# Kernel tuning notes

Measured on AMD Instinct MI355X. Metric: run time of the kernel, lower is better.

The kernel has to match this reference:

```python
import jax, jax.numpy as jnp
import numpy as np

DN = ('NCHW', 'OIHW', 'NCHW')
EPS = 1e-5


def _conv(x, w, b, stride, pad):
    y = jax.lax.conv_general_dilated(x, w, (stride, stride), ((pad, pad), (pad, pad)), dimension_numbers=DN)
    return y + b[None, :, None, None]


def _convT(x, w, b):
    # PyTorch ConvTranspose2d(k=3, stride=2, padding=1, output_padding=1)
    # weight w: [in, out, kh, kw] -> flip spatial, swap in/out -> OIHW
    wt = jnp.flip(w, (2, 3)).transpose(1, 0, 2, 3)
    y = jax.lax.conv_general_dilated(x, wt, (1, 1), ((1, 2), (1, 2)), lhs_dilation=(2, 2), dimension_numbers=DN)
    return y + b[None, :, None, None]


def _inorm(x):
    # InstanceNorm2d, affine=False, biased variance (num_features arg unused since no affine)
    m = x.mean((2, 3), keepdims=True)
    v = ((x - m) ** 2).mean((2, 3), keepdims=True)
    return (x - m) / jnp.sqrt(v + EPS)


def _lrelu(x):
    return jnp.where(x >= 0, x, 0.2 * x)


def _refpad(x):
    return jnp.pad(x, ((0, 0), (0, 0), (1, 1), (1, 1)), mode='reflect')


def _backbone(image, w1, b1, w2, b2, w3, b3, wt, bt, w4, b4):
    x = _lrelu(_inorm(_conv(_refpad(image), w1, b1, 1, 0)))   # [B,32,H,W]
    x = _lrelu(_inorm(_conv(x, w2, b2, 2, 1)))                 # [B,64,H/2,W/2]
    x = _lrelu(_inorm(_conv(x, w3, b3, 2, 1)))                 # [B,128,H/4,W/4]
    x = _lrelu(_inorm(_convT(x, wt, bt)))                      # [B,256,H/2,W/2]
    x = jnp.tanh(_conv(_refpad(x), w4, b4, 1, 0))              # [B,512,H/2,W/2]
    return x


def _style_codes(x, seg):
    # nearest interpolation of seg to (h,w): src_idx = floor(dst * H / h)
    B, C, h, w = x.shape
    H, W = seg.shape[2], seg.shape[3]
    rows = (np.arange(h) * H) // h
    cols = (np.arange(w) * W) // w
    seg_ds = seg[:, :, rows][:, :, :, cols]                    # [B,L,h,w]
    m = (seg_ds != 0).astype(x.dtype)
    sums = jnp.einsum('bchw,blhw->blc', x, m)                  # segment sums
    counts = m.sum((2, 3))[..., None]                          # [B,L,1]
    return jnp.where(counts > 0, sums / jnp.maximum(counts, 1.0), 0.0)


def setup_inputs():
    key = jax.random.key(0)
    ks = jax.random.split(key, 8)
    B, H, W, L = 8, 256, 256, 19
    image = jax.random.normal(ks[0], (B, 3, H, W), jnp.float32)
    labels = jax.random.randint(ks[1], (B, H, W), 0, L)
    seg = jax.nn.one_hot(labels, L, axis=1, dtype=jnp.float32)  # one-hot semantic map
    def w(k, shape):
        return jax.random.normal(k, shape, jnp.float32) * 0.05
    return {
        'image': image, 'seg': seg,
        'w1': w(ks[2], (32, 3, 3, 3)), 'b1': jnp.zeros(32, jnp.float32),
        'w2': w(ks[3], (64, 32, 3, 3)), 'b2': jnp.zeros(64, jnp.float32),
        'w3': w(ks[4], (128, 64, 3, 3)), 'b3': jnp.zeros(128, jnp.float32),
        'wt': w(ks[5], (128, 256, 3, 3)), 'bt': jnp.zeros(256, jnp.float32),
        'w4': w(ks[6], (512, 256, 3, 3)), 'b4': jnp.zeros(512, jnp.float32),
    }


def reference(image, seg, w1, b1, w2, b2, w3, b3, wt, bt, w4, b4):
    x = _backbone(image, w1, b1, w2, b2, w3, b3, wt, bt, w4, b4)
    return _style_codes(x, seg)  # [B, label_nc, 512]
```

## Files before the change

### kernel.cpp

```cpp
#include <hip/hip_runtime.h>
#include <hip/hip_bf16.h>
#include <math.h>

typedef __attribute__((ext_vector_type(8))) short bf16x8;
typedef __attribute__((ext_vector_type(8))) unsigned short u16x8;
typedef __attribute__((ext_vector_type(4))) float f32x4;
typedef __attribute__((ext_vector_type(2))) long longx2;

#define OFF_X1   0ull
#define OFF_XQ8  0ull
#define OFF_X2   34080768ull
#define OFF_X3   51386368ull
#define OFF_Y4   60039168ull
#define OFF_WB8  127148032ull
#define OFF_WB2  129507328ull
#define OFF_WB3  129548288ull
#define OFF_WBT  129695744ull
#define OFF_ST1  130744320ull
#define OFF_ST2  130746368ull
#define OFF_ST3  130750464ull
#define OFF_ST4  130758656ull
#define OFF_SUMS 130775040ull
#define OFF_CNT  131086336ull
#define OFF_LAB  131117664ull
#define OFF_DWS  131641952ull
#define OFF_WSM  132166240ull
#define OFF_ST5  132690528ull
#define OFF_CB   132706912ull

__device__ __forceinline__ float bfu2f(unsigned short u) {
  return __builtin_bit_cast(float, ((unsigned)u) << 16);
}
__device__ __forceinline__ unsigned short f2bfu(float f) {
  __hip_bfloat16 h = __float2bfloat16(f);
  return __builtin_bit_cast(unsigned short, h);
}
__device__ __forceinline__ void gload_lds16(const void* g, void* l) {
  __builtin_amdgcn_global_load_lds(
      (const __attribute__((address_space(1))) unsigned int*)g,
      (__attribute__((address_space(3))) unsigned int*)l, 16, 0, 0);
}
template <bool HI>
__device__ __forceinline__ int cvtpk8(float a, float b, int old) {
  return __builtin_amdgcn_cvt_pk_fp8_f32(a, b, old, HI);
}
template <int SEL>
__device__ __forceinline__ float cvtf8(int v) {
  return __builtin_amdgcn_cvt_f32_fp8(v, SEL);
}

#define WAITV(N) asm volatile("s_waitcnt vmcnt(" #N ")" ::: "memory")

#define PIPE_STEP(WAITN, BUF, DOSTAGE, SNEXT)                 \
  asm volatile("s_waitcnt vmcnt(" #WAITN ")" ::: "memory");   \
  __builtin_amdgcn_s_barrier();                               \
  __builtin_amdgcn_sched_barrier(0);                          \
  mmaStep(BUF, (BUF) + 16384);                                \
  __builtin_amdgcn_sched_barrier(0);                          \
  __builtin_amdgcn_s_barrier();                               \
  if (DOSTAGE) stage(SNEXT, BUF);

__device__ const int c_taptab[16] = {4, -1, -1, -1, 5, 3, -1, -1, 7, -1, 1, -1, 8, 6, 2, 0};

__global__ __launch_bounds__(256) void prep_k(
    const float* __restrict__ w2, unsigned short* __restrict__ wb2,
    const float* __restrict__ w3, unsigned short* __restrict__ wb3,
    const float* __restrict__ wt, unsigned short* __restrict__ wbt,
    const float* __restrict__ w4, unsigned char* __restrict__ wb8,
    float* __restrict__ dws, float* __restrict__ wsum,
    unsigned short* __restrict__ x1, unsigned short* __restrict__ x2,
    unsigned short* __restrict__ x3,
    const float* __restrict__ seg, int* __restrict__ lab, float* __restrict__ counts) {
  __shared__ int hist[19];
  int blk = blockIdx.x, t = threadIdx.x;
  if (blk < 80) {
    int idx = blk * 256 + t;
    if (idx < 20480) {
      int oc = idx / 320, r = idx % 320, tap = r >> 5, ic = r & 31;
      wb2[idx] = tap < 9 ? f2bfu(w2[(oc * 32 + ic) * 9 + tap]) : (unsigned short)0;
    }
  } else if (blk < 368) {
    int idx = (blk - 80) * 256 + t;
    int oc = idx / 576, r = idx % 576, tap = r >> 6, ic = r & 63;
    wb3[idx] = f2bfu(w3[(oc * 64 + ic) * 9 + tap]);
  } else if (blk < 2416) {
    int idx = (blk - 368) * 256 + t;
    int n = idx >> 9, k = idx & 511;
    int cl = n >> 8, oc = n & 255, nb = k >> 7, ic = k & 127;
    int tap = c_taptab[cl * 4 + nb];
    wbt[idx] = tap < 0 ? (unsigned short)0 : f2bfu(wt[(ic * 256 + oc) * 9 + tap]);
  } else if (blk < 2928) {
    int oc = blk - 2416, ic = t;
    int local = ic & 127;
    int p = (ic & 128) + ((local >> 3) & 3) * 32 + ((local >> 5) & 3) * 8 + (local & 7);
    float ds = 0.f, ws = 0.f;
    for (int kk = 0; kk < 9; ++kk) {
      float w = w4[(size_t)oc * 2304 + ic * 9 + kk];
      int pk = cvtpk8<false>(w, 0.f, 0);
      wb8[((size_t)oc * 9 + kk) * 256 + p] = (unsigned char)(pk & 0xff);
      float wq = cvtf8<0>(pk);
      ds += wq - w; ws += w;
    }
    dws[oc * 256 + ic] = ds;
    wsum[oc * 256 + ic] = ws;
  } else if (blk < 3252) {
    int u = (blk - 2928) * 256 + t;
    int b = u / 10368, r = u % 10368;
    u16x8 z = {0, 0, 0, 0, 0, 0, 0, 0};
    if (r < 4128) {
      unsigned short* base = x1 + (size_t)b * 2130048;
      if (r < 2064) {
        int row = r < 1032 ? 0 : 257, pos = r < 1032 ? r : r - 1032;
        base += (row * 258 + (pos >> 2)) * 32 + (pos & 3) * 8;
      } else {
        int rc = r - 2064;
        int col = rc < 1032 ? 0 : 257, pos = rc < 1032 ? rc : rc - 1032;
        base += ((pos >> 2) * 258 + col) * 32 + (pos & 3) * 8;
      }
      *(u16x8*)base = z;
    } else if (r < 8288) {
      int s = r - 4128;
      unsigned short* base = x2 + (size_t)b * 1081600;
      if (s < 2080) {
        int row = s < 1040 ? 0 : 129, pos = s < 1040 ? s : s - 1040;
        base += (row * 130 + (pos >> 3)) * 64 + (pos & 7) * 8;
      } else {
        int sc = s - 2080;
        int col = sc < 1040 ? 0 : 129, pos = sc < 1040 ? sc : sc - 1040;
        base += ((pos >> 3) * 130 + col) * 64 + (pos & 7) * 8;
      }
      *(u16x8*)base = z;
    } else {
      int tt = r - 8288;
      unsigned short* base = x3 + (size_t)b * 540800;
      if (tt < 1040) {
        base += (64 * 65 + (tt >> 4)) * 128 + (tt & 15) * 8;
      } else {
        int pos = tt - 1040;
        base += ((pos >> 4) * 65 + 64) * 128 + (pos & 15) * 8;
      }
      *(u16x8*)base = z;
    }
  } else {
    int blk2 = blk - 3252;
    int b = blk2 >> 6;
    int p = (blk2 & 63) * 256 + t;
    if (t < 19) hist[t] = 0;
    __syncthreads();
    int i = p >> 7, j = p & 127;
    const float* sp = seg + (size_t)b * 19 * 65536 + (2 * i) * 256 + 2 * j;
    int l = 0;
    for (int k = 0; k < 19; ++k) { if (sp[(size_t)k * 65536] != 0.f) { l = k; break; } }
    lab[b * 16384 + p] = l;
    atomicAdd(&hist[l], 1);
    __syncthreads();
    if (t < 19) atomicAdd(&counts[b * 19 + t], (float)hist[t]);
  }
}

__global__ __launch_bounds__(256) void conv1_k(const float* __restrict__ img,
                                               const float* __restrict__ w1,
                                               unsigned short* __restrict__ x1,
                                               float* __restrict__ st1) {
  __shared__ float wl[864];
  __shared__ float tile[256][33];
  __shared__ float cbins[64];
  int t = threadIdx.x, y = blockIdx.x, b = blockIdx.y;
  for (int i = t; i < 864; i += 256) wl[i] = w1[(i & 31) * 27 + (i >> 5)];
  if (t < 64) cbins[t] = 0.f;
  __syncthreads();
  int x = t;
  float val[27];
  for (int ic = 0; ic < 3; ++ic) {
    const float* ip = img + ((size_t)(b * 3 + ic)) * 65536;
#pragma unroll
    for (int ky = 0; ky < 3; ++ky) {
      int gy = y - 1 + ky; gy = gy < 0 ? -gy : (gy > 255 ? 510 - gy : gy);
#pragma unroll
      for (int kx = 0; kx < 3; ++kx) {
        int gx = x - 1 + kx; gx = gx < 0 ? -gx : (gx > 255 ? 510 - gx : gx);
        val[ic * 9 + ky * 3 + kx] = ip[gy * 256 + gx];
      }
    }
  }
  float a[32];
#pragma unroll
  for (int oc = 0; oc < 32; ++oc) a[oc] = 0.f;
#pragma unroll
  for (int k = 0; k < 27; ++k) {
    float vv = val[k];
#pragma unroll
    for (int oc = 0; oc < 32; ++oc) a[oc] += wl[k * 32 + oc] * vv;
  }
  unsigned short ov[32];
#pragma unroll
  for (int oc = 0; oc < 32; ++oc) ov[oc] = f2bfu(a[oc]);
  unsigned short* op = x1 + ((size_t)(b * 258 + y + 1) * 258 + (x + 1)) * 32;
#pragma unroll
  for (int i = 0; i < 4; ++i) *(u16x8*)(op + i * 8) = *(const u16x8*)(ov + i * 8);

#pragma unroll
  for (int oc = 0; oc < 32; ++oc) tile[t][oc] = a[oc];
  __syncthreads();
  int ch = t & 31, seg = t >> 5;
  float s = 0.f, q = 0.f;
  for (int r = 0; r < 32; ++r) {
    float v = tile[seg * 32 + ((r + seg) & 31)][ch];
    s += v; q += v * v;
  }
  atomicAdd(&cbins[ch * 2], s);
  atomicAdd(&cbins[ch * 2 + 1], q);
  __syncthreads();
  if (t < 64) atomicAdd(&st1[b * 64 + t], cbins[t]);
}

template <int C>
__global__ void nln_k(unsigned short* __restrict__ base, int rowStride, int unitsPerRow,
                      long bStride, const float* __restrict__ st, float invN) {
  const int CH8 = C / 8;
  int row = blockIdx.x, b = blockIdx.y;
  unsigned short* rp = base + (size_t)b * bStride + (size_t)row * rowStride;
  int ch = (threadIdx.x & (CH8 - 1)) * 8;
  const float* stb = st + b * C * 2;
  float2 m0[8];
#pragma unroll
  for (int e = 0; e < 8; ++e) {
    float m = stb[(ch + e) * 2] * invN;
    float v = stb[(ch + e) * 2 + 1] * invN - m * m;
    m0[e] = make_float2(m, rsqrtf(fmaxf(v, 0.f) + 1e-5f));
  }
  for (int idx = threadIdx.x; idx < unitsPerRow; idx += 256) {
    u16x8 v = *(u16x8*)(rp + idx * 8);
    u16x8 o;
#pragma unroll
    for (int e = 0; e < 8; ++e) {
      float f = (bfu2f(v[e]) - m0[e].x) * m0[e].y;
      o[e] = f2bfu(f >= 0.f ? f : 0.2f * f);
    }
    *(u16x8*)(rp + idx * 8) = o;
  }
}

__global__ __launch_bounds__(256) void nln8_k(const unsigned short* __restrict__ y4,
                                              const float* __restrict__ st4,
                                              unsigned char* __restrict__ xq8,
                                              float* __restrict__ st5) {
  __shared__ float bs[512];
  int t = threadIdx.x, row = blockIdx.x, b = blockIdx.y;
  int cg = t & 31, pg = t >> 5;
  int wof0 = (cg >> 4) * 128 + ((((cg & 15) & 3) << 2) | ((cg & 15) >> 2)) * 8;
  const float* stb = st4 + b * 512;
  const float invN = 1.f / 16384.f;
  float2 m0[8];
#pragma unroll
  for (int e = 0; e < 8; ++e) {
    float m = stb[(cg * 8 + e) * 2] * invN;
    float v = stb[(cg * 8 + e) * 2 + 1] * invN - m * m;
    m0[e] = make_float2(m, rsqrtf(fmaxf(v, 0.f) + 1e-5f));
  }
  const unsigned short* rp = y4 + ((size_t)b * 16384 + row * 128) * 256;
  unsigned char* op = xq8 + ((size_t)b * 16384 + (size_t)row * 128) * 256;
  float s[8] = {0, 0, 0, 0, 0, 0, 0, 0}, d[8] = {0, 0, 0, 0, 0, 0, 0, 0};
  for (int i = 0; i < 16; ++i) {
    int px = pg * 16 + i;
    u16x8 v = *(const u16x8*)(rp + (size_t)px * 256 + cg * 8);
    float f[8];
#pragma unroll
    for (int e = 0; e < 8; ++e) {
      float x = (bfu2f(v[e]) - m0[e].x) * m0[e].y;
      f[e] = x >= 0.f ? x : 0.2f * x;
    }
    int lo = cvtpk8<false>(f[0], f[1], 0); lo = cvtpk8<true>(f[2], f[3], lo);
    int hi = cvtpk8<false>(f[4], f[5], 0); hi = cvtpk8<true>(f[6], f[7], hi);
    *(long*)(op + (size_t)px * 256 + wof0) =
        ((long)(unsigned)hi << 32) | (unsigned)lo;
    float fq;
    fq = cvtf8<0>(lo); s[0] += fq; d[0] += fq - f[0];
    fq = cvtf8<1>(lo); s[1] += fq; d[1] += fq - f[1];
    fq = cvtf8<2>(lo); s[2] += fq; d[2] += fq - f[2];
    fq = cvtf8<3>(lo); s[3] += fq; d[3] += fq - f[3];
    fq = cvtf8<0>(hi); s[4] += fq; d[4] += fq - f[4];
    fq = cvtf8<1>(hi); s[5] += fq; d[5] += fq - f[5];
    fq = cvtf8<2>(hi); s[6] += fq; d[6] += fq - f[6];
    fq = cvtf8<3>(hi); s[7] += fq; d[7] += fq - f[7];
  }
  for (int i = t; i < 512; i += 256) bs[i] = 0.f;
  __syncthreads();
#pragma unroll
  for (int e = 0; e < 8; ++e) {
    atomicAdd(&bs[cg * 8 + e], s[e]);
    atomicAdd(&bs[256 + cg * 8 + e], d[e]);
  }
  __syncthreads();
  for (int i = t; i < 512; i += 256) atomicAdd(&st5[b * 512 + i], bs[i]);
}

__global__ __launch_bounds__(256) void cbias_k(const float* __restrict__ st5,
                                               const float* __restrict__ dws,
                                               const float* __restrict__ wsum,
                                               float* __restrict__ cb) {
  int oc = blockIdx.x, b = blockIdx.y, t = threadIdx.x;
  const float inv = 1.f / 16384.f;
  float muq = st5[b * 512 + t] * inv;
  float dmu = st5[b * 512 + 256 + t] * inv;
  float a = muq * dws[oc * 256 + t] + dmu * wsum[oc * 256 + t];
#pragma unroll
  for (int o = 1; o < 64; o <<= 1) a += __shfl_xor(a, o);
  __shared__ float r[4];
  if ((t & 63) == 0) r[t >> 6] = a;
  __syncthreads();
  if (t == 0) cb[b * 512 + oc] = r[0] + r[1] + r[2] + r[3];
}

__global__ __launch_bounds__(256) void conv2_k(const unsigned short* __restrict__ x1,
                                               const unsigned short* __restrict__ wb2,
                                               unsigned short* __restrict__ x2,
                                               float* __restrict__ st2) {
  __shared__ char smem[49664];
  float* bins = (float*)(smem + 49152);
  int tid = threadIdx.x, y = blockIdx.x, b = blockIdx.y;
  int lane = tid & 63, w = tid >> 6, wm = w >> 1, wn = w & 1;
  int lr = lane & 15, lg = lane >> 4;
  f32x4 acc[4][2];
#pragma unroll
  for (int i = 0; i < 4; ++i)
#pragma unroll
    for (int j = 0; j < 2; ++j) acc[i][j] = (f32x4){0.f, 0.f, 0.f, 0.f};

  int rowA[4], lcA[4], PbA[4];
#pragma unroll
  for (int i = 0; i < 4; ++i) {
    int pb = i * 256 + tid;
    PbA[i] = pb * 16; rowA[i] = pb >> 3; lcA[i] = (pb & 7) ^ (rowA[i] & 7);
  }
  int rowB[2], lcB[2], PbB[2];
#pragma unroll
  for (int i = 0; i < 2; ++i) {
    int pb = i * 256 + tid;
    PbB[i] = pb * 16; rowB[i] = pb >> 3; lcB[i] = (pb & 7) ^ (rowB[i] & 7);
  }
  const unsigned short* xb = x1 + (size_t)b * 2130048;

  auto stage = [&](int kb, char* base) {
    char* As = base;
    char* Bs = base + 16384;
#pragma unroll
    for (int i = 0; i < 4; ++i) {
      int tp = kb * 2 + (lcA[i] >> 2);
      int ky = (tp * 11) >> 5;
      int kx = tp - ky * 3;
      gload_lds16(xb + ((size_t)((2 * y + ky) * 258 + 2 * rowA[i] + kx)) * 32 + (lcA[i] & 3) * 8,
                  As + PbA[i]);
    }
#pragma unroll
    for (int i = 0; i < 2; ++i)
      gload_lds16(wb2 + rowB[i] * 320 + kb * 64 + lcB[i] * 8, Bs + PbB[i]);
  };

  stage(0, smem);
  __syncthreads();
  for (int kb = 0; kb < 5; ++kb) {
    char* base = smem + (kb & 1) * 24576;
    if (kb + 1 < 5) stage(kb + 1, smem + ((kb + 1) & 1) * 24576);
    char* As = base;
    char* Bs = base + 16384;
    bf16x8 af[4][2], bfr[2][2];
#pragma unroll
    for (int mi = 0; mi < 4; ++mi)
#pragma unroll
      for (int kh = 0; kh < 2; ++kh) {
        int row = wm * 64 + mi * 16 + lr;
        int byte = row * 128 + ((kh * 64 + lg * 16) ^ ((row & 7) << 4));
        af[mi][kh] = *(const bf16x8*)(As + byte);
      }
#pragma unroll
    for (int ni = 0; ni < 2; ++ni)
#pragma unroll
      for (int kh = 0; kh < 2; ++kh) {
        int row = wn * 32 + ni * 16 + lr;
        int byte = row * 128 + ((kh * 64 + lg * 16) ^ ((row & 7) << 4));
        bfr[ni][kh] = *(const bf16x8*)(Bs + byte);
      }
#pragma unroll
    for (int mi = 0; mi < 4; ++mi)
#pragma unroll
      for (int ni = 0; ni < 2; ++ni)
#pragma unroll
        for (int kh = 0; kh < 2; ++kh)
          acc[mi][ni] = __builtin_amdgcn_mfma_f32_16x16x32_bf16(af[mi][kh], bfr[ni][kh],
                                                                acc[mi][ni], 0, 0, 0);
    __syncthreads();
  }

  if (tid < 128) bins[tid] = 0.f;
  __syncthreads();
  unsigned short* ob = x2 + (size_t)b * 1081600;
#pragma unroll
  for (int ni = 0; ni < 2; ++ni) {
    int oc = wn * 32 + ni * 16 + lr;
    float s = 0.f, q = 0.f;
#pragma unroll
    for (int mi = 0; mi < 4; ++mi)
#pragma unroll
      for (int r = 0; r < 4; ++r) {
        int m = wm * 64 + mi * 16 + lg * 4 + r;
        float v = acc[mi][ni][r];
        ob[((y + 1) * 130 + m + 1) * 64 + oc] = f2bfu(v);
        s += v; q += v * v;
      }
    atomicAdd(&bins[oc * 2], s);
    atomicAdd(&bins[oc * 2 + 1], q);
  }
  __syncthreads();
  if (tid < 128) atomicAdd(&st2[b * 128 + tid], bins[tid]);
}

__global__ __launch_bounds__(256) void conv3_k(const unsigned short* __restrict__ x2,
                                               const unsigned short* __restrict__ wb3,
                                               unsigned short* __restrict__ x3,
                                               float* __restrict__ st3) {
  __shared__ char smem[66560];
  float* bins = (float*)(smem + 65536);
  int tid = threadIdx.x, y0 = blockIdx.x * 2, b = blockIdx.y;
  int lane = tid & 63, w = tid >> 6, wm = w >> 1, wn = w & 1;
  int lr = lane & 15, lg = lane >> 4;
  f32x4 acc[4][4];
#pragma unroll
  for (int i = 0; i < 4; ++i)
#pragma unroll
    for (int j = 0; j < 4; ++j) acc[i][j] = (f32x4){0.f, 0.f, 0.f, 0.f};

  int rowS[4], lc[4], Pb[4];
#pragma unroll
  for (int i = 0; i < 4; ++i) {
    int pb = i * 256 + tid;
    Pb[i] = pb * 16; rowS[i] = pb >> 3; lc[i] = (pb & 7) ^ (rowS[i] & 7);
  }
  const unsigned short* xb = x2 + (size_t)b * 1081600;

  auto stage = [&](int kk, char* base) {
    int ky = kk / 3, kx = kk - ky * 3;
#pragma unroll
    for (int i = 0; i < 4; ++i) {
      int m = rowS[i], di = m >> 6, xx = m & 63;
      gload_lds16(xb + ((size_t)((2 * (y0 + di) + ky) * 130 + 2 * xx + kx)) * 64 + lc[i] * 8,
                  base + Pb[i]);
    }
#pragma unroll
    for (int i = 0; i < 4; ++i)
      gload_lds16(wb3 + (rowS[i] * 9 + kk) * 64 + lc[i] * 8, base + 16384 + Pb[i]);
  };

  stage(0, smem);
  __syncthreads();
  for (int kk = 0; kk < 9; ++kk) {
    char* base = smem + (kk & 1) * 32768;
    if (kk + 1 < 9) stage(kk + 1, smem + ((kk + 1) & 1) * 32768);
    char* As = base;
    char* Bs = base + 16384;
    bf16x8 af[4][2], bfr[4][2];
#pragma unroll
    for (int mi = 0; mi < 4; ++mi)
#pragma unroll
      for (int kh = 0; kh < 2; ++kh) {
        int row = wm * 64 + mi * 16 + lr;
        int byte = row * 128 + ((kh * 64 + lg * 16) ^ ((row & 7) << 4));
        af[mi][kh] = *(const bf16x8*)(As + byte);
      }
#pragma unroll
    for (int ni = 0; ni < 4; ++ni)
#pragma unroll
      for (int kh = 0; kh < 2; ++kh) {
        int row = wn * 64 + ni * 16 + lr;
        int byte = row * 128 + ((kh * 64 + lg * 16) ^ ((row & 7) << 4));
        bfr[ni][kh] = *(const bf16x8*)(Bs + byte);
      }
#pragma unroll
    for (int mi = 0; mi < 4; ++mi)
#pragma unroll
      for (int ni = 0; ni < 4; ++ni)
#pragma unroll
        for (int kh = 0; kh < 2; ++kh)
          acc[mi][ni] = __builtin_amdgcn_mfma_f32_16x16x32_bf16(af[mi][kh], bfr[ni][kh],
                                                                acc[mi][ni], 0, 0, 0);
    __syncthreads();
  }

  if (tid < 256) bins[tid] = 0.f;
  __syncthreads();
  unsigned short* ob = x3 + (size_t)b * 540800;
#pragma unroll
  for (int ni = 0; ni < 4; ++ni) {
    int oc = wn * 64 + ni * 16 + lr;
    float s = 0.f, q = 0.f;
#pragma unroll
    for (int mi = 0; mi < 4; ++mi)
#pragma unroll
      for (int r = 0; r < 4; ++r) {
        int m = wm * 64 + mi * 16 + lg * 4 + r;
        int di = m >> 6, xx = m & 63;
        float v = acc[mi][ni][r];
        ob[((y0 + di) * 65 + xx) * 128 + oc] = f2bfu(v);
        s += v; q += v * v;
      }
    atomicAdd(&bins[oc * 2], s);
    atomicAdd(&bins[oc * 2 + 1], q);
  }
  __syncthreads();
  if (tid < 256) atomicAdd(&st3[b * 256 + tid], bins[tid]);
}

__global__ __launch_bounds__(256) void convT_k(const unsigned short* __restrict__ x3,
                                               const unsigned short* __restrict__ wbt,
                                               unsigned short* __restrict__ y4,
                                               float* __restrict__ st4) {
  __shared__ char smem[67584];
  float* bins = (float*)(smem + 65536);
  int tid = threadIdx.x, i0 = blockIdx.x * 2, nblk = blockIdx.y, b = blockIdx.z;
  int n0 = nblk * 128, cl = nblk >> 1, och0 = (nblk & 1) * 128;
  int lane = tid & 63, w = tid >> 6, wm = w >> 1, wn = w & 1;
  int lr = lane & 15, lg = lane >> 4;
  f32x4 acc[4][4];
#pragma unroll
  for (int i = 0; i < 4; ++i)
#pragma unroll
    for (int j = 0; j < 4; ++j) acc[i][j] = (f32x4){0.f, 0.f, 0.f, 0.f};

  int rowS[4], lc[4], Pb[4];
#pragma unroll
  for (int i = 0; i < 4; ++i) {
    int pb = i * 256 + tid;
    Pb[i] = pb * 16; rowS[i] = pb >> 3; lc[i] = (pb & 7) ^ (rowS[i] & 7);
  }
  int aoff[4][2], boff[4][2];
#pragma unroll
  for (int mi = 0; mi < 4; ++mi)
#pragma unroll
    for (int kh = 0; kh < 2; ++kh) {
      int row = wm * 64 + mi * 16 + lr;
      aoff[mi][kh] = row * 128 + ((kh * 64 + lg * 16) ^ ((row & 7) << 4));
      int rowb = wn * 64 + mi * 16 + lr;
      boff[mi][kh] = rowb * 128 + ((kh * 64 + lg * 16) ^ ((rowb & 7) << 4));
    }
  const unsigned short* xb = x3 + (size_t)b * 540800;

  auto stage = [&](int kb, char* base) {
    int nb = kb >> 1, chalf = (kb & 1) * 64;
#pragma unroll
    for (int i = 0; i < 4; ++i) {
      int m = rowS[i], di = m >> 6, j = m & 63;
      int pi = i0 + di + (nb >> 1), pj = j + (nb & 1);
      gload_lds16(xb + ((size_t)(pi * 65 + pj)) * 128 + chalf + lc[i] * 8, base + Pb[i]);
    }
#pragma unroll
    for (int i = 0; i < 4; ++i)
      gload_lds16(wbt + (size_t)(n0 + rowS[i]) * 512 + kb * 64 + lc[i] * 8,
                  base + 16384 + Pb[i]);
  };

  auto mmaStep = [&](char* As, char* Bs) {
    bf16x8 af[4][2], bfr[4][2];
#pragma unroll
    for (int mi = 0; mi < 4; ++mi)
#pragma unroll
      for (int kh = 0; kh < 2; ++kh) af[mi][kh] = *(const bf16x8*)(As + aoff[mi][kh]);
#pragma unroll
    for (int ni = 0; ni < 4; ++ni)
#pragma unroll
      for (int kh = 0; kh < 2; ++kh) bfr[ni][kh] = *(const bf16x8*)(Bs + boff[ni][kh]);
#pragma unroll
    for (int mi = 0; mi < 4; ++mi)
#pragma unroll
      for (int ni = 0; ni < 4; ++ni)
#pragma unroll
        for (int kh = 0; kh < 2; ++kh)
          acc[mi][ni] = __builtin_amdgcn_mfma_f32_16x16x32_bf16(af[mi][kh], bfr[ni][kh],
                                                                acc[mi][ni], 0, 0, 0);
  };

  char* B0 = smem;
  char* B1 = smem + 32768;
  stage(0, B0);
  stage(1, B1);
  for (int sp = 0; sp < 3; ++sp) {
    PIPE_STEP(8, B0, true, 2 * sp + 2);
    PIPE_STEP(8, B1, true, 2 * sp + 3);
  }
  PIPE_STEP(8, B0, false, 0);
  PIPE_STEP(0, B1, false, 0);

  if (tid < 256) bins[tid] = 0.f;
  __syncthreads();
  unsigned short* ob = y4 + (size_t)b * 4194304;
  int dy = cl >> 1, dx = cl & 1;
#pragma unroll
  for (int ni = 0; ni < 4; ++ni) {
    int loc = wn * 64 + ni * 16 + lr;
    int oc = och0 + loc;
    float s = 0.f, q = 0.f;
#pragma unroll
    for (int mi = 0; mi < 4; ++mi)
#pragma unroll
      for (int r = 0; r < 4; ++r) {
        int m = wm * 64 + mi * 16 + lg * 4 + r;
        int di = m >> 6, j = m & 63;
        int oy = 2 * (i0 + di) + dy, ox = 2 * j + dx;
        float v = acc[mi][ni][r];
        ob[(oy * 128 + ox) * 256 + oc] = f2bfu(v);
        s += v; q += v * v;
      }
    atomicAdd(&bins[loc * 2], s);
    atomicAdd(&bins[loc * 2 + 1], q);
  }
  __syncthreads();
  if (tid < 256) atomicAdd(&st4[b * 512 + och0 * 2 + tid], bins[tid]);
}

__global__ __launch_bounds__(256, 4) void conv4_k(
    const unsigned char* __restrict__ xq8, const unsigned char* __restrict__ wb8,
    const float* __restrict__ b4, const float* __restrict__ cb,
    const int* __restrict__ lab, float* __restrict__ sums) {
  __shared__ char smem[33280];
  char* As = smem;
  char* Bs = smem + 16384;
  int* labs = (int*)(smem + 32768);
  int tid = threadIdx.x;
  int id = blockIdx.x;
  int b = id & 7, rr = id >> 3;
  int y = rr >> 2, nblk = rr & 3;
  int n0 = nblk * 128;
  if (tid < 128) labs[tid] = lab[b * 16384 + y * 128 + tid];
  int lane = tid & 63, w = tid >> 6;
  int wm = w >> 1, wn = w & 1;
  int lr = lane & 15, lg = lane >> 4;

  f32x4 acc[4][4];
#pragma unroll
  for (int i = 0; i < 4; ++i)
#pragma unroll
    for (int j = 0; j < 4; ++j) acc[i][j] = (f32x4){0.f, 0.f, 0.f, 0.f};

  const unsigned char* xb = xq8 + (size_t)b * 4194304;

  int rs0 = tid >> 3;
  int csw = ((tid & 7) ^ (rs0 & 7)) << 4;
  int ldoff = tid * 16;

  const unsigned char* brow[4];
#pragma unroll
  for (int i = 0; i < 4; ++i)
    brow[i] = wb8 + (size_t)(n0 + rs0 + 32 * i) * 2304 + csw;

  int koff = 0;
  for (int kk = 0; kk < 9; ++kk) {
    int ky = (kk * 11) >> 5, kx = kk - ky * 3;
    int sy = y + ky - 1; sy = sy < 0 ? 1 : (sy > 127 ? 126 : sy);
    const unsigned char* arow[4];
#pragma unroll
    for (int i = 0; i < 4; ++i) {
      int sx = rs0 + 32 * i + kx - 1;
      sx = sx < 0 ? 1 : (sx > 127 ? 126 : sx);
      arow[i] = xb + ((size_t)(sy * 128 + sx)) * 256 + csw;
    }
    for (int ic0 = 0; ic0 < 256; ic0 += 128) {
      __syncthreads();
#pragma unroll
      for (int i = 0; i < 4; ++i) gload_lds16(arow[i] + ic0, As + i * 4096 + ldoff);
#pragma unroll
      for (int i = 0; i < 4; ++i) gload_lds16(brow[i] + koff, Bs + i * 4096 + ldoff);
      koff += 128;
      __syncthreads();

      longx2 bq[4][2];
#pragma unroll
      for (int ni = 0; ni < 4; ++ni) {
        int row = wn * 64 + ni * 16 + lr;
#pragma unroll
        for (int k2 = 0; k2 < 2; ++k2) {
          int byte = row * 128 + ((lg * 32 + k2 * 16) ^ ((row & 7) << 4));
          bq[ni][k2] = *(const longx2*)(Bs + byte);
        }
      }
#pragma unroll
      for (int mi = 0; mi < 4; ++mi) {
        int row = wm * 64 + mi * 16 + lr;
        longx2 aq[2];
#pragma unroll
        for (int k2 = 0; k2 < 2; ++k2) {
          int byte = row * 128 + ((lg * 32 + k2 * 16) ^ ((row & 7) << 4));
          aq[k2] = *(const longx2*)(As + byte);
        }
#pragma unroll
        for (int ni = 0; ni < 4; ++ni)
#pragma unroll
          for (int k2 = 0; k2 < 2; ++k2) {
            acc[mi][ni] = __builtin_amdgcn_mfma_f32_16x16x32_fp8_fp8(
                aq[k2][0], bq[ni][k2][0], acc[mi][ni], 0, 0, 0);
            acc[mi][ni] = __builtin_amdgcn_mfma_f32_16x16x32_fp8_fp8(
                aq[k2][1], bq[ni][k2][1], acc[mi][ni], 0, 0, 0);
          }
      }
    }
  }

  __syncthreads();
  float* bins = (float*)smem;
  for (int t2 = tid; t2 < 19 * 128; t2 += 256) bins[t2] = 0.f;
  __syncthreads();
  float bias[4];
#pragma unroll
  for (int ni = 0; ni < 4; ++ni) {
    int gc = n0 + wn * 64 + ni * 16 + lr;
    bias[ni] = b4[gc] - cb[b * 512 + gc];
  }
#pragma unroll
  for (int mi = 0; mi < 4; ++mi)
#pragma unroll
    for (int ni = 0; ni < 4; ++ni) {
      int ct = wn * 64 + ni * 16 + lr;
#pragma unroll
      for (int r = 0; r < 4; ++r) {
        int x = wm * 64 + mi * 16 + lg * 4 + r;
        float v = tanhf(acc[mi][ni][r] + bias[ni]);
        atomicAdd(&bins[labs[x] * 128 + ct], v);
      }
    }
  __syncthreads();
  for (int t2 = tid; t2 < 19 * 128; t2 += 256) {
    float v = bins[t2];
    if (v != 0.f)
      atomicAdd(&sums[((size_t)(b * 19 + (t2 >> 7))) * 512 + n0 + (t2 & 127)], v);
  }
}

__global__ void finalize_k(const float* __restrict__ sums, const float* __restrict__ counts,
                           float* __restrict__ out) {
  int idx = blockIdx.x * 256 + threadIdx.x;
  int bl = idx / 512;
  float c = counts[bl];
  out[idx] = c > 0.f ? sums[idx] / fmaxf(c, 1.f) : 0.f;
}

extern "C" void kernel_launch(void* const* d_in, const int* in_sizes, int n_in,
                              void* d_out, int out_size, void* d_ws, size_t ws_size,
                              hipStream_t stream) {
  const float* image = (const float*)d_in[0];
  const float* seg   = (const float*)d_in[1];
  const float* w1    = (const float*)d_in[2];
  const float* w2    = (const float*)d_in[4];
  const float* w3    = (const float*)d_in[6];
  const float* wt    = (const float*)d_in[8];
  const float* w4    = (const float*)d_in[10];
  const float* b4    = (const float*)d_in[11];
  float* out = (float*)d_out;
  char* ws = (char*)d_ws;

  unsigned short* x1  = (unsigned short*)(ws + OFF_X1);
  unsigned char*  xq8 = (unsigned char*)(ws + OFF_XQ8);
  unsigned short* x2  = (unsigned short*)(ws + OFF_X2);
  unsigned short* x3  = (unsigned short*)(ws + OFF_X3);
  unsigned short* y4  = (unsigned short*)(ws + OFF_Y4);
  unsigned char*  wb8 = (unsigned char*)(ws + OFF_WB8);
  unsigned short* wb2 = (unsigned short*)(ws + OFF_WB2);
  unsigned short* wb3 = (unsigned short*)(ws + OFF_WB3);
  unsigned short* wbt = (unsigned short*)(ws + OFF_WBT);
  float* st1 = (float*)(ws + OFF_ST1);
  float* st2 = (float*)(ws + OFF_ST2);
  float* st3 = (float*)(ws + OFF_ST3);
  float* st4 = (float*)(ws + OFF_ST4);
  float* sums = (float*)(ws + OFF_SUMS);
  float* counts = (float*)(ws + OFF_CNT);
  int* lab = (int*)(ws + OFF_LAB);
  float* dws  = (float*)(ws + OFF_DWS);
  float* wsum = (float*)(ws + OFF_WSM);
  float* st5  = (float*)(ws + OFF_ST5);
  float* cbv  = (float*)(ws + OFF_CB);

  hipMemsetAsync(ws + OFF_ST1, 0, 342624, stream);
  hipMemsetAsync(ws + OFF_ST5, 0, 16384, stream);
  prep_k<<<3764, 256, 0, stream>>>(w2, wb2, w3, wb3, wt, wbt, w4, wb8, dws, wsum,
                                   x1, x2, x3, seg, lab, counts);

  conv1_k<<<dim3(256, 8), 256, 0, stream>>>(image, w1, x1, st1);
  nln_k<32><<<dim3(256, 8), 256, 0, stream>>>(x1 + 259 * 32, 258 * 32, 1024, 2130048L,
                                              st1, 1.f / 65536.f);

  conv2_k<<<dim3(128, 8), 256, 0, stream>>>(x1, wb2, x2, st2);
  nln_k<64><<<dim3(128, 8), 256, 0, stream>>>(x2 + 131 * 64, 130 * 64, 1024, 1081600L,
                                              st2, 1.f / 16384.f);

  conv3_k<<<dim3(32, 8), 256, 0, stream>>>(x2, wb3, x3, st3);
  nln_k<128><<<dim3(64, 8), 256, 0, stream>>>(x3, 65 * 128, 1024, 540800L,
                                              st3, 1.f / 4096.f);

  convT_k<<<dim3(32, 8, 8), 256, 0, stream>>>(x3, wbt, y4, st4);

  nln8_k<<<dim3(128, 8), 256, 0, stream>>>(y4, st4, xq8, st5);
  cbias_k<<<dim3(512, 8), 256, 0, stream>>>(st5, dws, wsum, cbv);

  conv4_k<<<4096, 256, 0, stream>>>(xq8, wb8, b4, cbv, lab, sums);

  finalize_k<<<304, 256, 0, stream>>>(sums, counts, out);
}
```

Measured before the change: 691.5 us.

## Run transposed conv in FP8 MFMA with fused norm-and-quantize of x3

Replaces the bf16 transposed-convolution GEMM with an fp8 version. The x3 instance-norm+lrelu pass now writes a separate fp8 buffer laid out for the new kernel, and the convT weights are prepacked to fp8. The new kernel drops the double-buffered async pipeline for a simple load-then-compute loop over 4 K blocks, with half the LDS and a launch bound of 4 blocks per SIMD. This halves operand bytes and uses the faster fp8 MFMA, at the cost of lower precision and no load/compute overlap.

```diff
diff --git a/kernel.cpp b/kernel.cpp
--- a/kernel.cpp
+++ b/kernel.cpp
@@ -27,6 +27,7 @@
 #define OFF_WSM  132166240ull
 #define OFF_ST5  132690528ull
 #define OFF_CB   132706912ull
+#define OFF_X3Q  132723296ull
 
 __device__ __forceinline__ float bfu2f(unsigned short u) {
   return __builtin_bit_cast(float, ((unsigned)u) << 16);
@@ -49,27 +50,16 @@
   return __builtin_amdgcn_cvt_f32_fp8(v, SEL);
 }
 
-#define WAITV(N) asm volatile("s_waitcnt vmcnt(" #N ")" ::: "memory")
-
-#define PIPE_STEP(WAITN, BUF, DOSTAGE, SNEXT)                 \
-  asm volatile("s_waitcnt vmcnt(" #WAITN ")" ::: "memory");   \
-  __builtin_amdgcn_s_barrier();                               \
-  __builtin_amdgcn_sched_barrier(0);                          \
-  mmaStep(BUF, (BUF) + 16384);                                \
-  __builtin_amdgcn_sched_barrier(0);                          \
-  __builtin_amdgcn_s_barrier();                               \
-  if (DOSTAGE) stage(SNEXT, BUF);
-
 __device__ const int c_taptab[16] = {4, -1, -1, -1, 5, 3, -1, -1, 7, -1, 1, -1, 8, 6, 2, 0};
 
 __global__ __launch_bounds__(256) void prep_k(
     const float* __restrict__ w2, unsigned short* __restrict__ wb2,
     const float* __restrict__ w3, unsigned short* __restrict__ wb3,
-    const float* __restrict__ wt, unsigned short* __restrict__ wbt,
+    const float* __restrict__ wt, unsigned char* __restrict__ wbt8,
     const float* __restrict__ w4, unsigned char* __restrict__ wb8,
     float* __restrict__ dws, float* __restrict__ wsum,
     unsigned short* __restrict__ x1, unsigned short* __restrict__ x2,
-    unsigned short* __restrict__ x3,
+    unsigned char* __restrict__ x3q8,
     const float* __restrict__ seg, int* __restrict__ lab, float* __restrict__ counts) {
   __shared__ int hist[19];
   int blk = blockIdx.x, t = threadIdx.x;
@@ -88,7 +78,13 @@
     int n = idx >> 9, k = idx & 511;
     int cl = n >> 8, oc = n & 255, nb = k >> 7, ic = k & 127;
     int tap = c_taptab[cl * 4 + nb];
-    wbt[idx] = tap < 0 ? (unsigned short)0 : f2bfu(wt[(ic * 256 + oc) * 9 + tap]);
+    int p = ((ic >> 3) & 3) * 32 + ((ic >> 5) & 3) * 8 + (ic & 7);
+    unsigned char v = 0;
+    if (tap >= 0) {
+      int pk = cvtpk8<false>(wt[(ic * 256 + oc) * 9 + tap], 0.f, 0);
+      v = (unsigned char)(pk & 0xff);
+    }
+    wbt8[(size_t)n * 512 + nb * 128 + p] = v;
   } else if (blk < 2928) {
     int oc = blk - 2416, ic = t;
     int local = ic & 127;
@@ -103,46 +99,44 @@
     }
     dws[oc * 256 + ic] = ds;
     wsum[oc * 256 + ic] = ws;
-  } else if (blk < 3252) {
+  } else if (blk < 3220) {
     int u = (blk - 2928) * 256 + t;
-    int b = u / 10368, r = u % 10368;
-    u16x8 z = {0, 0, 0, 0, 0, 0, 0, 0};
-    if (r < 4128) {
-      unsigned short* base = x1 + (size_t)b * 2130048;
-      if (r < 2064) {
-        int row = r < 1032 ? 0 : 257, pos = r < 1032 ? r : r - 1032;
-        base += (row * 258 + (pos >> 2)) * 32 + (pos & 3) * 8;
+    if (u < 74560) {
+      int b = u / 9320, r = u % 9320;
+      u16x8 z = {0, 0, 0, 0, 0, 0, 0, 0};
+      if (r < 4128) {
+        unsigned short* base = x1 + (size_t)b * 2130048;
+        if (r < 2064) {
+          int row = r < 1032 ? 0 : 257, pos = r < 1032 ? r : r - 1032;
+          base += (row * 258 + (pos >> 2)) * 32 + (pos & 3) * 8;
+        } else {
+          int rc = r - 2064;
+          int col = rc < 1032 ? 0 : 257, pos = rc < 1032 ? rc : rc - 1032;
+          base += ((pos >> 2) * 258 + col) * 32 + (pos & 3) * 8;
+        }
+        *(u16x8*)base = z;
+      } else if (r < 8288) {
+        int s = r - 4128;
+        unsigned short* base = x2 + (size_t)b * 1081600;
+        if (s < 2080) {
+          int row = s < 1040 ? 0 : 129, pos = s < 1040 ? s : s - 1040;
+          base += (row * 130 + (pos >> 3)) * 64 + (pos & 7) * 8;
+        } else {
+          int sc = s - 2080;
+          int col = sc < 1040 ? 0 : 129, pos = sc < 1040 ? sc : sc - 1040;
+          base += ((pos >> 3) * 130 + col) * 64 + (pos & 7) * 8;
+        }
+        *(u16x8*)base = z;
       } else {
-        int rc = r - 2064;
-        int col = rc < 1032 ? 0 : 257, pos = rc < 1032 ? rc : rc - 1032;
-        base += ((pos >> 2) * 258 + col) * 32 + (pos & 3) * 8;
-      }
-      *(u16x8*)base = z;
-    } else if (r < 8288) {
-      int s = r - 4128;
-      unsigned short* base = x2 + (size_t)b * 1081600;
-      if (s < 2080) {
-        int row = s < 1040 ? 0 : 129, pos = s < 1040 ? s : s - 1040;
-        base += (row * 130 + (pos >> 3)) * 64 + (pos & 7) * 8;
-      } else {
-        int sc = s - 2080;
-        int col = sc < 1040 ? 0 : 129, pos = sc < 1040 ? sc : sc - 1040;
-        base += ((pos >> 3) * 130 + col) * 64 + (pos & 7) * 8;
-      }
-      *(u16x8*)base = z;
-    } else {
-      int tt = r - 8288;
-      unsigned short* base = x3 + (size_t)b * 540800;
-      if (tt < 1040) {
-        base += (64 * 65 + (tt >> 4)) * 128 + (tt & 15) * 8;
-      } else {
-        int pos = tt - 1040;
-        base += ((pos >> 4) * 65 + 64) * 128 + (pos & 15) * 8;
-      }
-      *(u16x8*)base = z;
+        int r3 = r - 8288;
+        int idx = r3 >> 3, un = r3 & 7;
+        int lin = idx < 65 ? (64 * 65 + idx) : ((idx - 65) * 65 + 64);
+        longx2 zz = {0, 0};
+        *(longx2*)(x3q8 + (size_t)b * 540800 + (size_t)lin * 128 + un * 16) = zz;
+      }
     }
   } else {
-    int blk2 = blk - 3252;
+    int blk2 = blk - 3220;
     int b = blk2 >> 6;
     int p = (blk2 & 63) * 256 + t;
     if (t < 19) hist[t] = 0;
@@ -238,6 +232,40 @@
       o[e] = f2bfu(f >= 0.f ? f : 0.2f * f);
     }
     *(u16x8*)(rp + idx * 8) = o;
+  }
+}
+
+__global__ __launch_bounds__(256) void x3cvt_k(const unsigned short* __restrict__ x3,
+                                               const float* __restrict__ st3,
+                                               unsigned char* __restrict__ x3q8) {
+  int t = threadIdx.x, i = blockIdx.x, b = blockIdx.y;
+  int cg = t & 15, pg = t >> 4;
+  int wof = ((((cg & 3) << 2) | (cg >> 2))) * 8;
+  const float* stb = st3 + b * 256;
+  const float invN = 1.f / 4096.f;
+  float2 m0[8];
+#pragma unroll
+  for (int e = 0; e < 8; ++e) {
+    float m = stb[(cg * 8 + e) * 2] * invN;
+    float v = stb[(cg * 8 + e) * 2 + 1] * invN - m * m;
+    m0[e] = make_float2(m, rsqrtf(fmaxf(v, 0.f) + 1e-5f));
+  }
+  const unsigned short* rp = x3 + (size_t)b * 540800;
+  unsigned char* op = x3q8 + (size_t)b * 540800;
+#pragma unroll
+  for (int jj = 0; jj < 4; ++jj) {
+    int j = pg * 4 + jj;
+    u16x8 v = *(const u16x8*)(rp + ((size_t)(i * 65 + j)) * 128 + cg * 8);
+    float f[8];
+#pragma unroll
+    for (int e = 0; e < 8; ++e) {
+      float x = (bfu2f(v[e]) - m0[e].x) * m0[e].y;
+      f[e] = x >= 0.f ? x : 0.2f * x;
+    }
+    int lo = cvtpk8<false>(f[0], f[1], 0); lo = cvtpk8<true>(f[2], f[3], lo);
+    int hi = cvtpk8<false>(f[4], f[5], 0); hi = cvtpk8<true>(f[6], f[7], hi);
+    *(long*)(op + ((size_t)(i * 65 + j)) * 128 + wof) =
+        ((long)(unsigned)hi << 32) | (unsigned)lo;
   }
 }
 
@@ -510,12 +538,14 @@
   if (tid < 256) atomicAdd(&st3[b * 256 + tid], bins[tid]);
 }
 
-__global__ __launch_bounds__(256) void convT_k(const unsigned short* __restrict__ x3,
-                                               const unsigned short* __restrict__ wbt,
-                                               unsigned short* __restrict__ y4,
-                                               float* __restrict__ st4) {
-  __shared__ char smem[67584];
-  float* bins = (float*)(smem + 65536);
+__global__ __launch_bounds__(256, 4) void convT8_k(const unsigned char* __restrict__ x3q8,
+                                                   const unsigned char* __restrict__ wbt8,
+                                                   unsigned short* __restrict__ y4,
+                                                   float* __restrict__ st4) {
+  __shared__ char smem[33792];
+  char* As = smem;
+  char* Bs = smem + 16384;
+  float* bins = (float*)(smem + 32768);
   int tid = threadIdx.x, i0 = blockIdx.x * 2, nblk = blockIdx.y, b = blockIdx.z;
   int n0 = nblk * 128, cl = nblk >> 1, och0 = (nblk & 1) * 128;
   int lane = tid & 63, w = tid >> 6, wm = w >> 1, wn = w & 1;
@@ -526,69 +556,58 @@
 #pragma unroll
     for (int j = 0; j < 4; ++j) acc[i][j] = (f32x4){0.f, 0.f, 0.f, 0.f};
 
-  int rowS[4], lc[4], Pb[4];
-#pragma unroll
-  for (int i = 0; i < 4; ++i) {
-    int pb = i * 256 + tid;
-    Pb[i] = pb * 16; rowS[i] = pb >> 3; lc[i] = (pb & 7) ^ (rowS[i] & 7);
-  }
-  int aoff[4][2], boff[4][2];
-#pragma unroll
-  for (int mi = 0; mi < 4; ++mi)
-#pragma unroll
-    for (int kh = 0; kh < 2; ++kh) {
+  int rs0 = tid >> 3;
+  int csw = ((tid & 7) ^ (rs0 & 7)) << 4;
+  int ldoff = tid * 16;
+  const unsigned char* xb = x3q8 + (size_t)b * 540800;
+
+  for (int nb = 0; nb < 4; ++nb) {
+    __syncthreads();
+#pragma unroll
+    for (int i = 0; i < 4; ++i) {
+      int m = rs0 + 32 * i, di = m >> 6, j = m & 63;
+      int pi = i0 + di + (nb >> 1), pj = j + (nb & 1);
+      gload_lds16(xb + ((size_t)(pi * 65 + pj)) * 128 + csw, As + i * 4096 + ldoff);
+    }
+#pragma unroll
+    for (int i = 0; i < 4; ++i) {
+      int n = rs0 + 32 * i;
+      gload_lds16(wbt8 + (size_t)(n0 + n) * 512 + nb * 128 + csw, Bs + i * 4096 + ldoff);
+    }
+    __syncthreads();
+
+    longx2 bq[4][2];
+#pragma unroll
+    for (int ni = 0; ni < 4; ++ni) {
+      int row = wn * 64 + ni * 16 + lr;
+#pragma unroll
+      for (int k2 = 0; k2 < 2; ++k2) {
+        int byte = row * 128 + ((lg * 32 + k2 * 16) ^ ((row & 7) << 4));
+        bq[ni][k2] = *(const longx2*)(Bs + byte);
+      }
+    }
+#pragma unroll
+    for (int mi = 0; mi < 4; ++mi) {
       int row = wm * 64 + mi * 16 + lr;
-      aoff[mi][kh] = row * 128 + ((kh * 64 + lg * 16) ^ ((row & 7) << 4));
-      int rowb = wn * 64 + mi * 16 + lr;
-      boff[mi][kh] = rowb * 128 + ((kh * 64 + lg * 16) ^ ((rowb & 7) << 4));
-    }
-  const unsigned short* xb = x3 + (size_t)b * 540800;
-
-  auto stage = [&](int kb, char* base) {
-    int nb = kb >> 1, chalf = (kb & 1) * 64;
-#pragma unroll
-    for (int i = 0; i < 4; ++i) {
-      int m = rowS[i], di = m >> 6, j = m & 63;
-      int pi = i0 + di + (nb >> 1), pj = j + (nb & 1);
-      gload_lds16(xb + ((size_t)(pi * 65 + pj)) * 128 + chalf + lc[i] * 8, base + Pb[i]);
-    }
-#pragma unroll
-    for (int i = 0; i < 4; ++i)
-      gload_lds16(wbt + (size_t)(n0 + rowS[i]) * 512 + kb * 64 + lc[i] * 8,
-                  base + 16384 + Pb[i]);
-  };
-
-  auto mmaStep = [&](char* As, char* Bs) {
-    bf16x8 af[4][2], bfr[4][2];
-#pragma unroll
-    for (int mi = 0; mi < 4; ++mi)
-#pragma unroll
-      for (int kh = 0; kh < 2; ++kh) af[mi][kh] = *(const bf16x8*)(As + aoff[mi][kh]);
-#pragma unroll
-    for (int ni = 0; ni < 4; ++ni)
-#pragma unroll
-      for (int kh = 0; kh < 2; ++kh) bfr[ni][kh] = *(const bf16x8*)(Bs + boff[ni][kh]);
-#pragma unroll
-    for (int mi = 0; mi < 4; ++mi)
+      longx2 aq[2];
+#pragma unroll
+      for (int k2 = 0; k2 < 2; ++k2) {
+        int byte = row * 128 + ((lg * 32 + k2 * 16) ^ ((row & 7) << 4));
+        aq[k2] = *(const longx2*)(As + byte);
+      }
 #pragma unroll
       for (int ni = 0; ni < 4; ++ni)
 #pragma unroll
-        for (int kh = 0; kh < 2; ++kh)
-          acc[mi][ni] = __builtin_amdgcn_mfma_f32_16x16x32_bf16(af[mi][kh], bfr[ni][kh],
-                                                                acc[mi][ni], 0, 0, 0);
-  };
-
-  char* B0 = smem;
-  char* B1 = smem + 32768;
-  stage(0, B0);
-  stage(1, B1);
-  for (int sp = 0; sp < 3; ++sp) {
-    PIPE_STEP(8, B0, true, 2 * sp + 2);
-    PIPE_STEP(8, B1, true, 2 * sp + 3);
-  }
-  PIPE_STEP(8, B0, false, 0);
-  PIPE_STEP(0, B1, false, 0);
-
+        for (int k2 = 0; k2 < 2; ++k2) {
+          acc[mi][ni] = __builtin_amdgcn_mfma_f32_16x16x32_fp8_fp8(
+              aq[k2][0], bq[ni][k2][0], acc[mi][ni], 0, 0, 0);
+          acc[mi][ni] = __builtin_amdgcn_mfma_f32_16x16x32_fp8_fp8(
+              aq[k2][1], bq[ni][k2][1], acc[mi][ni], 0, 0, 0);
+        }
+    }
+  }
+
+  __syncthreads();
   if (tid < 256) bins[tid] = 0.f;
   __syncthreads();
   unsigned short* ob = y4 + (size_t)b * 4194304;
@@ -755,15 +774,16 @@
   float* out = (float*)d_out;
   char* ws = (char*)d_ws;
 
-  unsigned short* x1  = (unsigned short*)(ws + OFF_X1);
-  unsigned char*  xq8 = (unsigned char*)(ws + OFF_XQ8);
-  unsigned short* x2  = (unsigned short*)(ws + OFF_X2);
-  unsigned short* x3  = (unsigned short*)(ws + OFF_X3);
-  unsigned short* y4  = (unsigned short*)(ws + OFF_Y4);
-  unsigned char*  wb8 = (unsigned char*)(ws + OFF_WB8);
-  unsigned short* wb2 = (unsigned short*)(ws + OFF_WB2);
-  unsigned short* wb3 = (unsigned short*)(ws + OFF_WB3);
-  unsigned short* wbt = (unsigned short*)(ws + OFF_WBT);
+  unsigned short* x1   = (unsigned short*)(ws + OFF_X1);
+  unsigned char*  xq8  = (unsigned char*)(ws + OFF_XQ8);
+  unsigned short* x2   = (unsigned short*)(ws + OFF_X2);
+  unsigned short* x3   = (unsigned short*)(ws + OFF_X3);
+  unsigned char*  x3q8 = (unsigned char*)(ws + OFF_X3Q);
+  unsigned short* y4   = (unsigned short*)(ws + OFF_Y4);
+  unsigned char*  wb8  = (unsigned char*)(ws + OFF_WB8);
+  unsigned short* wb2  = (unsigned short*)(ws + OFF_WB2);
+  unsigned short* wb3  = (unsigned short*)(ws + OFF_WB3);
+  unsigned char*  wbt8 = (unsigned char*)(ws + OFF_WBT);
   float* st1 = (float*)(ws + OFF_ST1);
   float* st2 = (float*)(ws + OFF_ST2);
   float* st3 = (float*)(ws + OFF_ST3);
@@ -778,8 +798,8 @@
 
   hipMemsetAsync(ws + OFF_ST1, 0, 342624, stream);
   hipMemsetAsync(ws + OFF_ST5, 0, 16384, stream);
-  prep_k<<<3764, 256, 0, stream>>>(w2, wb2, w3, wb3, wt, wbt, w4, wb8, dws, wsum,
-                                   x1, x2, x3, seg, lab, counts);
+  prep_k<<<3732, 256, 0, stream>>>(w2, wb2, w3, wb3, wt, wbt8, w4, wb8, dws, wsum,
+                                   x1, x2, x3q8, seg, lab, counts);
 
   conv1_k<<<dim3(256, 8), 256, 0, stream>>>(image, w1, x1, st1);
   nln_k<32><<<dim3(256, 8), 256, 0, stream>>>(x1 + 259 * 32, 258 * 32, 1024, 2130048L,
@@ -790,10 +810,9 @@
                                               st2, 1.f / 16384.f);
 
   conv3_k<<<dim3(32, 8), 256, 0, stream>>>(x2, wb3, x3, st3);
-  nln_k<128><<<dim3(64, 8), 256, 0, stream>>>(x3, 65 * 128, 1024, 540800L,
-                                              st3, 1.f / 4096.f);
-
-  convT_k<<<dim3(32, 8, 8), 256, 0, stream>>>(x3, wbt, y4, st4);
+  x3cvt_k<<<dim3(64, 8), 256, 0, stream>>>(x3, st3, x3q8);
+
+  convT8_k<<<dim3(32, 8, 8), 256, 0, stream>>>(x3q8, wbt8, y4, st4);
 
   nln8_k<<<dim3(128, 8), 256, 0, stream>>>(y4, st4, xq8, st5);
   cbias_k<<<dim3(512, 8), 256, 0, stream>>>(st5, dws, wsum, cbv);
```

Result: no change. 679.6 us (-1.7%).
